# Performance work log

Measured on AMD Instinct MI355X. Metric: run time of the kernel, lower is better.

## Reference

```python
import jax, jax.numpy as jnp
import numpy as np

N_HEADS = 8
N_GROUPS = 32  # GroupNorm groups (normalization(channels) in guided-diffusion)
EPS = 1e-5


def setup_inputs() -> dict:
    key = jax.random.key(0)
    ks = jax.random.split(key, 7)
    b, c, hh, ww = 16, 512, 32, 32
    x = jax.random.normal(ks[0], (b, c, hh, ww), dtype=jnp.float32)
    norm_w = 1.0 + 0.02 * jax.random.normal(ks[1], (c,), dtype=jnp.float32)
    norm_b = 0.02 * jax.random.normal(ks[2], (c,), dtype=jnp.float32)
    # pointwise Conv1d == matmul over channels; note proj_out is zero-initialized
    # in the original, we use random weights so the op is non-trivial.
    qkv_w = jax.random.normal(ks[3], (3 * c, c), dtype=jnp.float32) / np.sqrt(c).astype(np.float32)
    qkv_b = 0.02 * jax.random.normal(ks[4], (3 * c,), dtype=jnp.float32)
    proj_w = jax.random.normal(ks[5], (c, c), dtype=jnp.float32) / np.sqrt(c).astype(np.float32)
    proj_b = 0.02 * jax.random.normal(ks[6], (c,), dtype=jnp.float32)
    return {"x": x, "norm_w": norm_w, "norm_b": norm_b,
            "qkv_w": qkv_w, "qkv_b": qkv_b, "proj_w": proj_w, "proj_b": proj_b}


def reference(x, norm_w, norm_b, qkv_w, qkv_b, proj_w, proj_b):
    b, c, hh, ww = x.shape
    t = hh * ww
    xf = x.reshape(b, c, t)

    # GroupNorm(32, c): normalize over (c//G channels, T) per group
    xg = xf.reshape(b, N_GROUPS, (c // N_GROUPS) * t)
    mu = jnp.mean(xg, axis=-1, keepdims=True)
    var = jnp.var(xg, axis=-1, keepdims=True)
    hn = ((xg - mu) * jax.lax.rsqrt(var + EPS)).reshape(b, c, t)
    hn = hn * norm_w[:, None] + norm_b[:, None]

    # pointwise conv: [b, 3c, t]
    qkv = jnp.einsum('oc,bct->bot', qkv_w, hn) + qkv_b[:, None]

    ch = c // N_HEADS
    qkv = qkv.reshape(b * N_HEADS, 3 * ch, t)
    q, k, v = jnp.split(qkv, 3, axis=1)  # each [b*H, ch, t]
    scale = np.float32(1.0 / np.sqrt(np.sqrt(ch)))
    w = jnp.einsum('bct,bcs->bts', q * scale, k * scale)  # [b*H, t, t]
    w = jax.nn.softmax(w.astype(jnp.float32), axis=-1).astype(qkv.dtype)
    a = jnp.einsum('bts,bcs->bct', w, v).reshape(b, c, t)

    h = jnp.einsum('oc,bct->bot', proj_w, a) + proj_b[:, None]
    return (xf + h).reshape(b, c, hh, ww)
```

## Files before the change

kernel.cpp:

```cpp
#include <hip/hip_runtime.h>

#define TPB 256

typedef __attribute__((ext_vector_type(8))) __bf16 bf16x8;
typedef __attribute__((ext_vector_type(4))) float f32x4;
typedef __attribute__((ext_vector_type(8))) unsigned short u16x8;
typedef __attribute__((ext_vector_type(4))) unsigned short u16x4;
typedef __attribute__((ext_vector_type(4))) unsigned int u32x4;
typedef __attribute__((ext_vector_type(2))) unsigned int u32x2;

typedef __attribute__((address_space(1))) const void gconst_void;
typedef __attribute__((address_space(3))) void lds_void;

__device__ __forceinline__ unsigned short f2bf(float f) {
  unsigned u = __builtin_bit_cast(unsigned, f);
  u += 0x7FFFu + ((u >> 16) & 1u);
  return (unsigned short)(u >> 16);
}

__device__ __forceinline__ float exp2_fast(float x) {
  float r;
  asm("v_exp_f32 %0, %1" : "=v"(r) : "v"(x));
  return r;
}

__device__ __forceinline__ float rcp_fast(float x) {
  float r;
  asm("v_rcp_f32 %0, %1" : "=v"(r) : "v"(x));
  return r;
}

__device__ __forceinline__ unsigned cvt_pk_bf16(float lo, float hi) {
  unsigned r;
  asm("v_cvt_pk_bf16_f32 %0, %1, %2" : "=v"(r) : "v"(lo), "v"(hi));
  return r;
}


__global__ __launch_bounds__(256) void k_gn_fused(const float* __restrict__ x,
                                                  const float* __restrict__ nw,
                                                  const float* __restrict__ nb,
                                                  unsigned short* __restrict__ hnT) {
  int bg = blockIdx.x;
  int b = bg >> 5, g = bg & 31;
  size_t base = (size_t)(b * 512 + g * 16) * 1024;
  const float4* p = reinterpret_cast<const float4*>(x + base);
  float s = 0.f, ss = 0.f;
#pragma unroll
  for (int i = 0; i < 16; ++i) {
    float4 v = p[threadIdx.x + i * 256];
    s += v.x + v.y + v.z + v.w;
    ss += v.x * v.x + v.y * v.y + v.z * v.z + v.w * v.w;
  }
#pragma unroll
  for (int off = 1; off < 64; off <<= 1) {
    s += __shfl_xor(s, off, 64);
    ss += __shfl_xor(ss, off, 64);
  }
  __shared__ float rbuf[4][2];
  __shared__ float stat[2];
  int wave = threadIdx.x >> 6;
  if ((threadIdx.x & 63) == 0) { rbuf[wave][0] = s; rbuf[wave][1] = ss; }
  __syncthreads();
  if (threadIdx.x == 0) {
    float S = 0.f, SS = 0.f;
    for (int i = 0; i < 4; ++i) { S += rbuf[i][0]; SS += rbuf[i][1]; }
    float m = S * (1.f / 16384.f);
    float var = SS * (1.f / 16384.f) - m * m;
    stat[0] = m;
    stat[1] = rsqrtf(var + 1e-5f);
  }
  __syncthreads();
  float mu = stat[0], rinv = stat[1];

  int tid = threadIdx.x;
#pragma unroll
  for (int q = 0; q < 2; ++q) {
    int c0 = g * 16 + q * 8;
    float a[8], bb[8];
#pragma unroll
    for (int cc = 0; cc < 8; ++cc) {
      a[cc] = rinv * nw[c0 + cc];
      bb[cc] = nb[c0 + cc] - mu * a[cc];
    }
    size_t cpart = (size_t)(c0 >> 5) * 512 + (size_t)((c0 >> 3) & 3) * 128;
#pragma unroll
    for (int it = 0; it < 4; ++it) {
      int t = it * 256 + tid;
      u16x8 o;
#pragma unroll
      for (int cc = 0; cc < 8; ++cc) {
        float v = x[base + (size_t)(q * 8 + cc) * 1024 + t];
        o[cc] = f2bf(v * a[cc] + bb[cc]);
      }
      size_t dst = (size_t)b * 524288 + (size_t)(t >> 4) * 8192 + cpart + (t & 15) * 8;
      *reinterpret_cast<u16x8*>(hnT + dst) = o;
    }
  }
}

__global__ void k_f32_to_bf16(const float* __restrict__ src, unsigned short* __restrict__ dst,
                              int n4) {
  int i = blockIdx.x * blockDim.x + threadIdx.x;
  if (i < n4) {
    float4 v = reinterpret_cast<const float4*>(src)[i];
    u16x4 o;
    o[0] = f2bf(v.x); o[1] = f2bf(v.y); o[2] = f2bf(v.z); o[3] = f2bf(v.w);
    reinterpret_cast<u16x4*>(dst)[i] = o;
  }
}

__global__ void k_pack_w(const float* __restrict__ src, unsigned short* __restrict__ dst,
                         int nchunks) {
  int i = blockIdx.x * blockDim.x + threadIdx.x;
  if (i >= nchunks) return;
  int r = i >> 6, k8 = i & 63;
  const float4* s = reinterpret_cast<const float4*>(src + (size_t)r * 512 + k8 * 8);
  float4 v0 = s[0], v1 = s[1];
  u16x8 o;
  o[0] = f2bf(v0.x); o[1] = f2bf(v0.y); o[2] = f2bf(v0.z); o[3] = f2bf(v0.w);
  o[4] = f2bf(v1.x); o[5] = f2bf(v1.y); o[6] = f2bf(v1.z); o[7] = f2bf(v1.w);
  size_t d = (size_t)(r >> 4) * 8192 + (size_t)(k8 >> 2) * 512 + (k8 & 3) * 128 + (r & 15) * 8;
  *reinterpret_cast<u16x8*>(dst + d) = o;
}

#define MFMAS(AF, BF)                                                                     \
  do {                                                                                    \
    _Pragma("unroll") for (int mi = 0; mi < 4; ++mi)                                      \
      _Pragma("unroll") for (int ni = 0; ni < 4; ++ni)                                    \
        acc[mi][ni] =                                                                     \
            __builtin_amdgcn_mfma_f32_16x16x32_bf16(AF[mi], BF[ni], acc[mi][ni], 0, 0, 0);\
  } while (0)

#define LOADT(DA, DB, kb)                                                                 \
  do {                                                                                    \
    _Pragma("unroll") for (int mi = 0; mi < 4; ++mi)                                      \
      DA[mi] = *reinterpret_cast<const bf16x8*>(pA + (size_t)mi * 8192 + (kb) * 512);     \
    _Pragma("unroll") for (int ni = 0; ni < 4; ++ni)                                      \
      DB[ni] = *reinterpret_cast<const bf16x8*>(pB + (size_t)ni * 8192 + (kb) * 512);     \
  } while (0)

__global__ __launch_bounds__(256, 2) void k_qkv_gemm(
    const unsigned short* __restrict__ hnT, const unsigned short* __restrict__ wq,
    const float* __restrict__ qkv_b, unsigned short* __restrict__ Q,
    unsigned short* __restrict__ Kq, unsigned short* __restrict__ Vq) {
  int tid = threadIdx.x;
  int lane = tid & 63, wave = tid >> 6;
  int wm = wave >> 1, wn = wave & 1;
  int g = lane >> 4, li = lane & 15;

  int wg = blockIdx.x;
  int lin = (wg & 7) * 192 + (wg >> 3);
  int bx = lin % 12;
  int tmp = lin / 12;
  int by = tmp & 7;
  int b = tmp >> 3;
  int mbase = by * 128;
  int nbase = bx * 128;

  const unsigned short* pA =
      hnT + (size_t)b * 524288 + (size_t)((mbase + wm * 64) >> 4) * 8192 + lane * 8;
  const unsigned short* pB = wq + (size_t)((nbase + wn * 64) >> 4) * 8192 + lane * 8;

  f32x4 zero = {0.f, 0.f, 0.f, 0.f};
  f32x4 acc[4][4];
#pragma unroll
  for (int mi = 0; mi < 4; ++mi)
#pragma unroll
    for (int ni = 0; ni < 4; ++ni) acc[mi][ni] = zero;

  bf16x8 a0[4], b0[4], a1[4], b1[4];
  LOADT(a0, b0, 0);
#pragma unroll
  for (int kb = 0; kb < 16; kb += 2) {
    if (kb + 1 < 16) LOADT(a1, b1, kb + 1);
    MFMAS(a0, b0);
    if (kb + 2 < 16) LOADT(a0, b0, kb + 2);
    MFMAS(a1, b1);
  }

  const float SCALE = 0.42466090143f;
#pragma unroll
  for (int ni = 0; ni < 4; ++ni) {
    int o = nbase + wn * 64 + ni * 16 + li;
    int h = o / 192;
    int j = o - h * 192;
    int bh = b * 8 + h;
    float bias = qkv_b[o];
#pragma unroll
    for (int mi = 0; mi < 4; ++mi) {
      int t0 = mbase + wm * 64 + mi * 16 + g * 4;
      f32x4 v = acc[mi][ni];
      if (j < 64) {
#pragma unroll
        for (int r = 0; r < 4; ++r)
          Q[((size_t)bh * 1024 + t0 + r) * 64 + j] = f2bf((v[r] + bias) * SCALE);
      } else if (j < 128) {
#pragma unroll
        for (int r = 0; r < 4; ++r)
          Kq[((size_t)bh * 1024 + t0 + r) * 64 + (j - 64)] = f2bf((v[r] + bias) * SCALE);
      } else {
        int ch = j - 128;
        int nj = ch >> 4, liv = ch & 15;
        int stile = t0 >> 6, s0 = t0 & 63;
        int kkc = s0 >> 5, gk = (s0 >> 3) & 3, e0 = s0 & 7;
        u16x4 pv;
#pragma unroll
        for (int r = 0; r < 4; ++r) pv[r] = f2bf(v[r] + bias);
        *reinterpret_cast<u16x4*>(Vq + (size_t)bh * 65536 + (size_t)stile * 4096 +
                                  nj * 1024 + kkc * 512 + gk * 128 + liv * 8 + e0) = pv;
      }
    }
  }
}

__global__ __launch_bounds__(256) void k_attn(
    const unsigned short* __restrict__ Q, const unsigned short* __restrict__ K,
    const unsigned short* __restrict__ Vp, unsigned short* __restrict__ aT) {
  __shared__ unsigned short Kls[2][8192];
  int tid = threadIdx.x;
  int lane = tid & 63, w = tid >> 6;
  int g = lane >> 4, li = lane & 15;

  int wg = blockIdx.x;
  int lin = (wg & 7) * 128 + (wg >> 3);
  int qt = lin & 7;
  int bh = lin >> 3;
  int tq0 = qt * 128;
  int b = bh >> 3, h = bh & 7;

  const unsigned short* Kg = K + (size_t)bh * 1024 * 64;
  const unsigned short* Vb = Vp + (size_t)bh * 65536 + lane * 8;

  bf16x8 qf[2][2];
#pragma unroll
  for (int qi = 0; qi < 2; ++qi) {
    int t = tq0 + w * 32 + qi * 16 + li;
    const unsigned short* qp = Q + ((size_t)bh * 1024 + t) * 64 + g * 8;
    qf[qi][0] = *reinterpret_cast<const bf16x8*>(qp);
    qf[qi][1] = *reinterpret_cast<const bf16x8*>(qp + 32);
  }

  const unsigned short* kg[4];
#pragma unroll
  for (int i = 0; i < 4; ++i) {
    int r = w * 32 + i * 8 + (lane >> 3);
    int hh = (r ^ (r >> 2)) & 7;
    int c = ((lane & 7) ^ hh) * 8;
    kg[i] = Kg + (size_t)r * 64 + c;
  }

  int srowK = ((li >> 2) << 3) | (li & 3);

  f32x4 zero = {0.f, 0.f, 0.f, 0.f};
  f32x4 oacc[2][4];
  f32x4 l_acc[2];
#pragma unroll
  for (int qi = 0; qi < 2; ++qi) {
    l_acc[qi] = zero;
#pragma unroll
    for (int nj = 0; nj < 4; ++nj) oacc[qi][nj] = zero;
  }
  u32x4 onesw = {0x3F803F80u, 0x3F803F80u, 0x3F803F80u, 0x3F803F80u};
  bf16x8 ones = __builtin_bit_cast(bf16x8, onesw);

#define ISSUE(pp, ph)                                                                    \
  do {                                                                                   \
    _Pragma("unroll") for (int i = 0; i < 4; ++i)                                        \
        __builtin_amdgcn_global_load_lds((gconst_void*)(kg[i] + (size_t)(ph) * 8192),    \
                                         (lds_void*)&Kls[pp][w * 2048 + i * 512], 16, 0, \
                                         0);                                             \
  } while (0)

  ISSUE(0, 0);
  for (int ph = 0; ph < 8; ++ph) {
    asm volatile("s_waitcnt vmcnt(0) lgkmcnt(0)" ::: "memory");
    __builtin_amdgcn_s_barrier();
    asm volatile("" ::: "memory");
    if (ph < 7) ISSUE((ph + 1) & 1, ph + 1);

#pragma unroll
    for (int st = 0; st < 2; ++st) {
      const unsigned short* kbase = &Kls[ph & 1][st * 4096];
      const unsigned short* vt = Vb + (size_t)(ph * 2 + st) * 4096;

      bf16x8 vf0[4];
#pragma unroll
      for (int i = 0; i < 4; ++i) vf0[i] = *reinterpret_cast<const bf16x8*>(vt + i * 512);

      f32x4 sacc[2][4];
      __builtin_amdgcn_s_setprio(1);
#pragma unroll
      for (int ni = 0; ni < 4; ++ni) {
        int rK = ((ni >> 1) << 5) + ((ni & 1) << 2) + srowK;
        int hs = ((rK ^ (rK >> 2)) & 7) << 4;
        int off0 = ((g << 4)) ^ hs;
        int off1 = (64 + (g << 4)) ^ hs;
        bf16x8 kf0 = *reinterpret_cast<const bf16x8*>(&kbase[rK * 64 + (off0 >> 1)]);
        bf16x8 kf1 = *reinterpret_cast<const bf16x8*>(&kbase[rK * 64 + (off1 >> 1)]);
#pragma unroll
        for (int qi = 0; qi < 2; ++qi) {
          f32x4 s0 = __builtin_amdgcn_mfma_f32_16x16x32_bf16(kf0, qf[qi][0], zero, 0, 0, 0);
          sacc[qi][ni] = __builtin_amdgcn_mfma_f32_16x16x32_bf16(kf1, qf[qi][1], s0, 0, 0, 0);
        }
      }
      __builtin_amdgcn_s_setprio(0);

      bf16x8 pfrag[2][2];
#pragma unroll
      for (int qi = 0; qi < 2; ++qi) {
#pragma unroll
        for (int ni = 0; ni < 4; ++ni)
#pragma unroll
          for (int r = 0; r < 4; ++r) sacc[qi][ni][r] = exp2_fast(sacc[qi][ni][r]);
#pragma unroll
        for (int kk = 0; kk < 2; ++kk) {
          u32x4 pw;
          pw[0] = cvt_pk_bf16(sacc[qi][2 * kk][0], sacc[qi][2 * kk][1]);
          pw[1] = cvt_pk_bf16(sacc[qi][2 * kk][2], sacc[qi][2 * kk][3]);
          pw[2] = cvt_pk_bf16(sacc[qi][2 * kk + 1][0], sacc[qi][2 * kk + 1][1]);
          pw[3] = cvt_pk_bf16(sacc[qi][2 * kk + 1][2], sacc[qi][2 * kk + 1][3]);
          pfrag[qi][kk] = __builtin_bit_cast(bf16x8, pw);
        }
        l_acc[qi] = __builtin_amdgcn_mfma_f32_16x16x32_bf16(ones, pfrag[qi][0], l_acc[qi], 0, 0, 0);
        l_acc[qi] = __builtin_amdgcn_mfma_f32_16x16x32_bf16(ones, pfrag[qi][1], l_acc[qi], 0, 0, 0);
      }

      bf16x8 vf1[4];
#pragma unroll
      for (int i = 0; i < 4; ++i)
        vf1[i] = *reinterpret_cast<const bf16x8*>(vt + (4 + i) * 512);

      __builtin_amdgcn_s_setprio(1);
#pragma unroll
      for (int nj = 0; nj < 2; ++nj)
#pragma unroll
        for (int qi = 0; qi < 2; ++qi) {
          oacc[qi][nj] = __builtin_amdgcn_mfma_f32_16x16x32_bf16(vf0[nj * 2 + 0], pfrag[qi][0], oacc[qi][nj], 0, 0, 0);
          oacc[qi][nj] = __builtin_amdgcn_mfma_f32_16x16x32_bf16(vf0[nj * 2 + 1], pfrag[qi][1], oacc[qi][nj], 0, 0, 0);
        }
#pragma unroll
      for (int nj = 2; nj < 4; ++nj)
#pragma unroll
        for (int qi = 0; qi < 2; ++qi) {
          oacc[qi][nj] = __builtin_amdgcn_mfma_f32_16x16x32_bf16(vf1[(nj - 2) * 2 + 0], pfrag[qi][0], oacc[qi][nj], 0, 0, 0);
          oacc[qi][nj] = __builtin_amdgcn_mfma_f32_16x16x32_bf16(vf1[(nj - 2) * 2 + 1], pfrag[qi][1], oacc[qi][nj], 0, 0, 0);
        }
      __builtin_amdgcn_s_setprio(0);
    }
  }
#undef ISSUE

#pragma unroll
  for (int qi = 0; qi < 2; ++qi) {
    float inv = rcp_fast(l_acc[qi][0]);
    int t = tq0 + w * 32 + qi * 16 + li;
#pragma unroll
    for (int nj = 0; nj < 4; ++nj) {
      u32x2 ov;
      ov[0] = cvt_pk_bf16(oacc[qi][nj][0] * inv, oacc[qi][nj][1] * inv);
      ov[1] = cvt_pk_bf16(oacc[qi][nj][2] * inv, oacc[qi][nj][3] * inv);
      *reinterpret_cast<u32x2*>(aT + ((size_t)b * 1024 + t) * 512 + h * 64 + nj * 16 + g * 4) = ov;
    }
  }
}

__global__ __launch_bounds__(256) void k_proj_gemm(
    const unsigned short* __restrict__ aT, const unsigned short* __restrict__ wp,
    const float* __restrict__ proj_b, const float* __restrict__ x,
    float* __restrict__ out) {
  __shared__ unsigned short As[2][4096];
  __shared__ unsigned short Bs[2][4096];
  int tid = threadIdx.x;
  int lane = tid & 63, wave = tid >> 6;
  int wm = wave >> 1, wn = wave & 1;
  int g = lane >> 4, li = lane & 15;

  int wg = blockIdx.x;
  int lin = (wg & 7) * 64 + (wg >> 3);
  int bx = lin & 7;
  int tmp = lin >> 3;
  int by = tmp & 3;
  int b = tmp >> 2;
  int mbase = by * 128;
  int nbase = bx * 128;

  const unsigned short* Ag = wp + (size_t)mbase * 512;
  const unsigned short* Bg = aT + (size_t)b * 1024 * 512 + (size_t)nbase * 512;

  int kq = (lane & 3) ^ ((lane >> 3) & 3);
  int rst = wave * 32 + (lane >> 2);
  const char* pA0 = (const char*)Ag + (size_t)rst * 1024 + kq * 16;
  const char* pA1 = pA0 + 16 * 1024;
  const char* pB0 = (const char*)Bg + (size_t)rst * 1024 + kq * 16;
  const char* pB1 = pB0 + 16 * 1024;
  int ldsA0 = wave * 1024, ldsA1 = wave * 1024 + 512;

  int voff = 32 * li + 8 * (g ^ ((li >> 1) & 3));

  f32x4 zero = {0.f, 0.f, 0.f, 0.f};
  f32x4 acc[4][4];
#pragma unroll
  for (int mi = 0; mi < 4; ++mi)
#pragma unroll
    for (int ni = 0; ni < 4; ++ni) acc[mi][ni] = zero;

#define GISSUE(k0, buf)                                                                  \
  do {                                                                                   \
    __builtin_amdgcn_global_load_lds((gconst_void*)(pA0 + (k0) * 2),                     \
                                     (lds_void*)&As[buf][ldsA0], 16, 0, 0);              \
    __builtin_amdgcn_global_load_lds((gconst_void*)(pA1 + (k0) * 2),                     \
                                     (lds_void*)&As[buf][ldsA1], 16, 0, 0);              \
    __builtin_amdgcn_global_load_lds((gconst_void*)(pB0 + (k0) * 2),                     \
                                     (lds_void*)&Bs[buf][ldsA0], 16, 0, 0);              \
    __builtin_amdgcn_global_load_lds((gconst_void*)(pB1 + (k0) * 2),                     \
                                     (lds_void*)&Bs[buf][ldsA1], 16, 0, 0);              \
  } while (0)

  GISSUE(0, 0);
#pragma unroll
  for (int kk = 0; kk < 16; ++kk) {
    asm volatile("s_waitcnt vmcnt(0)" ::: "memory");
    __builtin_amdgcn_s_barrier();
    asm volatile("" ::: "memory");
    if (kk < 15) GISSUE((kk + 1) * 32, (kk + 1) & 1);
    const int cur = kk & 1;
    bf16x8 af[4], bfr[4];
#pragma unroll
    for (int mi = 0; mi < 4; ++mi)
      af[mi] = *reinterpret_cast<const bf16x8*>(&As[cur][wm * 2048 + mi * 512 + voff]);
#pragma unroll
    for (int ni = 0; ni < 4; ++ni)
      bfr[ni] = *reinterpret_cast<const bf16x8*>(&Bs[cur][wn * 2048 + ni * 512 + voff]);
#pragma unroll
    for (int mi = 0; mi < 4; ++mi)
#pragma unroll
      for (int ni = 0; ni < 4; ++ni)
        acc[mi][ni] = __builtin_amdgcn_mfma_f32_16x16x32_bf16(af[mi], bfr[ni], acc[mi][ni], 0, 0, 0);
  }
#undef GISSUE

#pragma unroll
  for (int mi = 0; mi < 4; ++mi) {
#pragma unroll
    for (int ni = 0; ni < 4; ++ni) {
      int t = nbase + wn * 64 + ni * 16 + li;
      f32x4 v = acc[mi][ni];
#pragma unroll
      for (int r = 0; r < 4; ++r) {
        int o = mbase + wm * 64 + mi * 16 + g * 4 + r;
        size_t idx = ((size_t)(b * 512 + o)) * 1024 + t;
        out[idx] = v[r] + proj_b[o] + x[idx];
      }
    }
  }
}

extern "C" void kernel_launch(void* const* d_in, const int* in_sizes, int n_in,
                              void* d_out, int out_size, void* d_ws, size_t ws_size,
                              hipStream_t stream) {
  (void)in_sizes; (void)n_in; (void)out_size; (void)ws_size;
  const float* x = (const float*)d_in[0];
  const float* norm_w = (const float*)d_in[1];
  const float* norm_b = (const float*)d_in[2];
  const float* qkv_w = (const float*)d_in[3];
  const float* qkv_b = (const float*)d_in[4];
  const float* proj_w = (const float*)d_in[5];
  const float* proj_b = (const float*)d_in[6];
  float* out = (float*)d_out;

  char* ws = (char*)d_ws;
  size_t off = 0;
  unsigned short* hnT = (unsigned short*)(ws + off); off += (size_t)16 * 1024 * 512 * 2;
  unsigned short* wqb = (unsigned short*)(ws + off); off += (size_t)1536 * 512 * 2;
  unsigned short* wpb = (unsigned short*)(ws + off); off += (size_t)512 * 512 * 2;
  unsigned short* Qb = (unsigned short*)(ws + off); off += (size_t)128 * 1024 * 64 * 2;
  unsigned short* Kb = (unsigned short*)(ws + off); off += (size_t)128 * 1024 * 64 * 2;
  unsigned short* Vb = (unsigned short*)(ws + off); off += (size_t)128 * 1024 * 64 * 2;

  k_gn_fused<<<512, TPB, 0, stream>>>(x, norm_w, norm_b, hnT);
  k_pack_w<<<(98304 + TPB - 1) / TPB, TPB, 0, stream>>>(qkv_w, wqb, 98304);
  k_f32_to_bf16<<<(262144 / 4 + TPB - 1) / TPB, TPB, 0, stream>>>(proj_w, wpb, 262144 / 4);
  k_qkv_gemm<<<1536, TPB, 0, stream>>>(hnT, wqb, qkv_b, Qb, Kb, Vb);
  k_attn<<<1024, TPB, 0, stream>>>(Qb, Kb, Vb, hnT );
  k_proj_gemm<<<512, TPB, 0, stream>>>(hnT, wpb, proj_b, x, out);
}
```

Measured before the change: 126.1 us.

## Split attention block into eight waves of sixteen queries each

The attention kernel now launches 512 threads per block instead of 256. Each of eight waves handles 16 query rows rather than each of four waves handling 32. Per-wave accumulators and score registers are halved, and the K tile load into LDS is spread across twice as many waves. The aim is more resident waves to hide memory and exp latency. In exchange, each V fragment and K LDS read is reused for only one query tile instead of two, which doubles V global reads and K LDS reads per block.

```diff
diff --git a/kernel.cpp b/kernel.cpp
--- a/kernel.cpp
+++ b/kernel.cpp
@@ -214,7 +214,7 @@
   }
 }
 
-__global__ __launch_bounds__(256) void k_attn(
+__global__ __launch_bounds__(512) void k_attn(
     const unsigned short* __restrict__ Q, const unsigned short* __restrict__ K,
     const unsigned short* __restrict__ Vp, unsigned short* __restrict__ aT) {
   __shared__ unsigned short Kls[2][8192];
@@ -232,19 +232,18 @@
   const unsigned short* Kg = K + (size_t)bh * 1024 * 64;
   const unsigned short* Vb = Vp + (size_t)bh * 65536 + lane * 8;
 
-  bf16x8 qf[2][2];
-#pragma unroll
-  for (int qi = 0; qi < 2; ++qi) {
-    int t = tq0 + w * 32 + qi * 16 + li;
+  bf16x8 qf[2];
+  {
+    int t = tq0 + w * 16 + li;
     const unsigned short* qp = Q + ((size_t)bh * 1024 + t) * 64 + g * 8;
-    qf[qi][0] = *reinterpret_cast<const bf16x8*>(qp);
-    qf[qi][1] = *reinterpret_cast<const bf16x8*>(qp + 32);
-  }
-
-  const unsigned short* kg[4];
-#pragma unroll
-  for (int i = 0; i < 4; ++i) {
-    int r = w * 32 + i * 8 + (lane >> 3);
+    qf[0] = *reinterpret_cast<const bf16x8*>(qp);
+    qf[1] = *reinterpret_cast<const bf16x8*>(qp + 32);
+  }
+
+  const unsigned short* kg[2];
+#pragma unroll
+  for (int i = 0; i < 2; ++i) {
+    int r = w * 16 + i * 8 + (lane >> 3);
     int hh = (r ^ (r >> 2)) & 7;
     int c = ((lane & 7) ^ hh) * 8;
     kg[i] = Kg + (size_t)r * 64 + c;
@@ -253,22 +252,18 @@
   int srowK = ((li >> 2) << 3) | (li & 3);
 
   f32x4 zero = {0.f, 0.f, 0.f, 0.f};
-  f32x4 oacc[2][4];
-  f32x4 l_acc[2];
-#pragma unroll
-  for (int qi = 0; qi < 2; ++qi) {
-    l_acc[qi] = zero;
-#pragma unroll
-    for (int nj = 0; nj < 4; ++nj) oacc[qi][nj] = zero;
-  }
+  f32x4 oacc[4];
+  f32x4 l_acc = zero;
+#pragma unroll
+  for (int nj = 0; nj < 4; ++nj) oacc[nj] = zero;
   u32x4 onesw = {0x3F803F80u, 0x3F803F80u, 0x3F803F80u, 0x3F803F80u};
   bf16x8 ones = __builtin_bit_cast(bf16x8, onesw);
 
 #define ISSUE(pp, ph)                                                                    \
   do {                                                                                   \
-    _Pragma("unroll") for (int i = 0; i < 4; ++i)                                        \
+    _Pragma("unroll") for (int i = 0; i < 2; ++i)                                        \
         __builtin_amdgcn_global_load_lds((gconst_void*)(kg[i] + (size_t)(ph) * 8192),    \
-                                         (lds_void*)&Kls[pp][w * 2048 + i * 512], 16, 0, \
+                                         (lds_void*)&Kls[pp][w * 1024 + i * 512], 16, 0, \
                                          0);                                             \
   } while (0)
 
@@ -288,7 +283,7 @@
 #pragma unroll
       for (int i = 0; i < 4; ++i) vf0[i] = *reinterpret_cast<const bf16x8*>(vt + i * 512);
 
-      f32x4 sacc[2][4];
+      f32x4 sacc[4];
       __builtin_amdgcn_s_setprio(1);
 #pragma unroll
       for (int ni = 0; ni < 4; ++ni) {
@@ -298,33 +293,27 @@
         int off1 = (64 + (g << 4)) ^ hs;
         bf16x8 kf0 = *reinterpret_cast<const bf16x8*>(&kbase[rK * 64 + (off0 >> 1)]);
         bf16x8 kf1 = *reinterpret_cast<const bf16x8*>(&kbase[rK * 64 + (off1 >> 1)]);
-#pragma unroll
-        for (int qi = 0; qi < 2; ++qi) {
-          f32x4 s0 = __builtin_amdgcn_mfma_f32_16x16x32_bf16(kf0, qf[qi][0], zero, 0, 0, 0);
-          sacc[qi][ni] = __builtin_amdgcn_mfma_f32_16x16x32_bf16(kf1, qf[qi][1], s0, 0, 0, 0);
-        }
+        f32x4 s0 = __builtin_amdgcn_mfma_f32_16x16x32_bf16(kf0, qf[0], zero, 0, 0, 0);
+        sacc[ni] = __builtin_amdgcn_mfma_f32_16x16x32_bf16(kf1, qf[1], s0, 0, 0, 0);
       }
       __builtin_amdgcn_s_setprio(0);
 
-      bf16x8 pfrag[2][2];
-#pragma unroll
-      for (int qi = 0; qi < 2; ++qi) {
-#pragma unroll
-        for (int ni = 0; ni < 4; ++ni)
-#pragma unroll
-          for (int r = 0; r < 4; ++r) sacc[qi][ni][r] = exp2_fast(sacc[qi][ni][r]);
-#pragma unroll
-        for (int kk = 0; kk < 2; ++kk) {
-          u32x4 pw;
-          pw[0] = cvt_pk_bf16(sacc[qi][2 * kk][0], sacc[qi][2 * kk][1]);
-          pw[1] = cvt_pk_bf16(sacc[qi][2 * kk][2], sacc[qi][2 * kk][3]);
-          pw[2] = cvt_pk_bf16(sacc[qi][2 * kk + 1][0], sacc[qi][2 * kk + 1][1]);
-          pw[3] = cvt_pk_bf16(sacc[qi][2 * kk + 1][2], sacc[qi][2 * kk + 1][3]);
-          pfrag[qi][kk] = __builtin_bit_cast(bf16x8, pw);
-        }
-        l_acc[qi] = __builtin_amdgcn_mfma_f32_16x16x32_bf16(ones, pfrag[qi][0], l_acc[qi], 0, 0, 0);
-        l_acc[qi] = __builtin_amdgcn_mfma_f32_16x16x32_bf16(ones, pfrag[qi][1], l_acc[qi], 0, 0, 0);
-      }
+      bf16x8 pfrag[2];
+#pragma unroll
+      for (int ni = 0; ni < 4; ++ni)
+#pragma unroll
+        for (int r = 0; r < 4; ++r) sacc[ni][r] = exp2_fast(sacc[ni][r]);
+#pragma unroll
+      for (int kk = 0; kk < 2; ++kk) {
+        u32x4 pw;
+        pw[0] = cvt_pk_bf16(sacc[2 * kk][0], sacc[2 * kk][1]);
+        pw[1] = cvt_pk_bf16(sacc[2 * kk][2], sacc[2 * kk][3]);
+        pw[2] = cvt_pk_bf16(sacc[2 * kk + 1][0], sacc[2 * kk + 1][1]);
+        pw[3] = cvt_pk_bf16(sacc[2 * kk + 1][2], sacc[2 * kk + 1][3]);
+        pfrag[kk] = __builtin_bit_cast(bf16x8, pw);
+      }
+      l_acc = __builtin_amdgcn_mfma_f32_16x16x32_bf16(ones, pfrag[0], l_acc, 0, 0, 0);
+      l_acc = __builtin_amdgcn_mfma_f32_16x16x32_bf16(ones, pfrag[1], l_acc, 0, 0, 0);
 
       bf16x8 vf1[4];
 #pragma unroll
@@ -333,33 +322,28 @@
 
       __builtin_amdgcn_s_setprio(1);
 #pragma unroll
-      for (int nj = 0; nj < 2; ++nj)
-#pragma unroll
-        for (int qi = 0; qi < 2; ++qi) {
-          oacc[qi][nj] = __builtin_amdgcn_mfma_f32_16x16x32_bf16(vf0[nj * 2 + 0], pfrag[qi][0], oacc[qi][nj], 0, 0, 0);
-          oacc[qi][nj] = __builtin_amdgcn_mfma_f32_16x16x32_bf16(vf0[nj * 2 + 1], pfrag[qi][1], oacc[qi][nj], 0, 0, 0);
-        }
-#pragma unroll
-      for (int nj = 2; nj < 4; ++nj)
-#pragma unroll
-        for (int qi = 0; qi < 2; ++qi) {
-          oacc[qi][nj] = __builtin_amdgcn_mfma_f32_16x16x32_bf16(vf1[(nj - 2) * 2 + 0], pfrag[qi][0], oacc[qi][nj], 0, 0, 0);
-          oacc[qi][nj] = __builtin_amdgcn_mfma_f32_16x16x32_bf16(vf1[(nj - 2) * 2 + 1], pfrag[qi][1], oacc[qi][nj], 0, 0, 0);
-        }
+      for (int nj = 0; nj < 2; ++nj) {
+        oacc[nj] = __builtin_amdgcn_mfma_f32_16x16x32_bf16(vf0[nj * 2 + 0], pfrag[0], oacc[nj], 0, 0, 0);
+        oacc[nj] = __builtin_amdgcn_mfma_f32_16x16x32_bf16(vf0[nj * 2 + 1], pfrag[1], oacc[nj], 0, 0, 0);
+      }
+#pragma unroll
+      for (int nj = 2; nj < 4; ++nj) {
+        oacc[nj] = __builtin_amdgcn_mfma_f32_16x16x32_bf16(vf1[(nj - 2) * 2 + 0], pfrag[0], oacc[nj], 0, 0, 0);
+        oacc[nj] = __builtin_amdgcn_mfma_f32_16x16x32_bf16(vf1[(nj - 2) * 2 + 1], pfrag[1], oacc[nj], 0, 0, 0);
+      }
       __builtin_amdgcn_s_setprio(0);
     }
   }
 #undef ISSUE
 
-#pragma unroll
-  for (int qi = 0; qi < 2; ++qi) {
-    float inv = rcp_fast(l_acc[qi][0]);
-    int t = tq0 + w * 32 + qi * 16 + li;
+  {
+    float inv = rcp_fast(l_acc[0]);
+    int t = tq0 + w * 16 + li;
 #pragma unroll
     for (int nj = 0; nj < 4; ++nj) {
       u32x2 ov;
-      ov[0] = cvt_pk_bf16(oacc[qi][nj][0] * inv, oacc[qi][nj][1] * inv);
-      ov[1] = cvt_pk_bf16(oacc[qi][nj][2] * inv, oacc[qi][nj][3] * inv);
+      ov[0] = cvt_pk_bf16(oacc[nj][0] * inv, oacc[nj][1] * inv);
+      ov[1] = cvt_pk_bf16(oacc[nj][2] * inv, oacc[nj][3] * inv);
       *reinterpret_cast<u32x2*>(aT + ((size_t)b * 1024 + t) * 512 + h * 64 + nj * 16 + g * 4) = ov;
     }
   }
@@ -482,6 +466,6 @@
   k_pack_w<<<(98304 + TPB - 1) / TPB, TPB, 0, stream>>>(qkv_w, wqb, 98304);
   k_f32_to_bf16<<<(262144 / 4 + TPB - 1) / TPB, TPB, 0, stream>>>(proj_w, wpb, 262144 / 4);
   k_qkv_gemm<<<1536, TPB, 0, stream>>>(hnT, wqb, qkv_b, Qb, Kb, Vb);
-  k_attn<<<1024, TPB, 0, stream>>>(Qb, Kb, Vb, hnT );
+  k_attn<<<1024, 512, 0, stream>>>(Qb, Kb, Vb, hnT );
   k_proj_gemm<<<512, TPB, 0, stream>>>(hnT, wpb, proj_b, x, out);
 }
```

Result: no change. 128.1 us (+1.6%).
